# Performance work log

Hardware: AMD Instinct MI355X
Metric: run time of the kernel (lower is better)

## Reference

```python
import jax, jax.numpy as jnp
import numpy as np

IN_CH, OUT_CH, K, STRIDE, PAD = 256, 256, 3, 1, 1

# Straight-through-estimator sign (torch Binarize: sign fwd, identity bwd)
@jax.custom_vjp
def ste_sign(x):
    return jnp.sign(x)

def _ste_fwd(x):
    return jnp.sign(x), None

def _ste_bwd(_, g):
    return (g,)

ste_sign.defvjp(_ste_fwd, _ste_bwd)


def setup_inputs() -> dict:
    key = jax.random.key(0)
    ks = jax.random.split(key, 4)
    x = jax.random.normal(ks[0], (32, IN_CH, 56, 56), jnp.float32)
    shift1 = jnp.zeros((1, IN_CH, 1, 1), jnp.float32)
    shift2 = jnp.zeros((1, IN_CH, 1, 1), jnp.float32)
    fan_in = IN_CH * K * K
    weight = jax.random.normal(ks[1], (OUT_CH, IN_CH, K, K), jnp.float32) / np.sqrt(fan_in)
    bias = jax.random.normal(ks[2], (OUT_CH,), jnp.float32) * 0.01
    w1 = jax.random.uniform(ks[3], (1,), jnp.float32) * 0.001  # channel_w scalar
    return {"x": x, "shift1": shift1, "shift2": shift2,
            "weight": weight, "bias": bias, "w1": w1}


def _binarize_conv2d(x, weight, bias):
    # BinarizeConv2d: binarize input (in_ch != 3) and weight via sign, fp conv, add bias
    xb = ste_sign(x)
    wb = ste_sign(weight)
    out = jax.lax.conv_general_dilated(
        xb, wb,
        window_strides=(STRIDE, STRIDE),
        padding=[(PAD, PAD), (PAD, PAD)],
        dimension_numbers=("NCHW", "OIHW", "NCHW"))
    return out + bias[None, :, None, None]


def reference(x, shift1, shift2, weight, bias, w1):
    out1 = _binarize_conv2d(x + shift1, weight, bias)
    out2 = _binarize_conv2d(x + shift2, weight, bias)
    return out1 + w1 * out2
```

## Files before the change

kernel.cpp:

```cpp
#include <hip/hip_runtime.h>
#include <stdint.h>

typedef __attribute__((ext_vector_type(4))) int   i32x4v;
typedef __attribute__((ext_vector_type(16))) int  i32x16v;
typedef __attribute__((ext_vector_type(4))) float f32x4;

#define PIX 3136
#define WW 56
#define SLAB 215296
#define APL 3712
#define WIN16 928
#define EPQ (32*69*4)
#define LDSB (4*EPQ)

#define XBP_BYTES ((size_t)32*4*3364*64)
#define OFF_XBP2  (XBP_BYTES)
#define OFF_WBT   (2*XBP_BYTES)
#define WBT_BYTES ((size_t)9*16*256*16)
#define OFF_FLAG  (OFF_WBT + WBT_BYTES)
#define WS_NEED   (OFF_FLAG + 64)

__global__ __launch_bounds__(256) void k_prep(
    const float* __restrict__ s1, const float* __restrict__ s2,
    const float* __restrict__ w, char* __restrict__ ws,
    char* __restrict__ wbTt, int* __restrict__ flag) {
    int b = blockIdx.x;
    int t = threadIdx.x;
    if (b == 0) {
        __shared__ int bad;
        if (t == 0) bad = 0;
        __syncthreads();
        if (s1[t] != s2[t]) atomicAdd(&bad, 1);
        __syncthreads();
        if (t == 0) *flag = (bad == 0) ? 1 : 0;
        return;
    }
    if (b <= 256) {
        char* base = ws + (size_t)(b - 1) * SLAB;
        int4 z = {0, 0, 0, 0};
#pragma unroll
        for (int i = 0; i < 4; ++i) {
            int u = t + i * 256;
            if (u >= 912) break;
            int off;
            if (u < 232)      off = u;
            else if (u < 464) off = 57 * 232 + (u - 232);
            else if (u < 688) { int r = (u - 464) >> 2; off = (r + 1) * 232 + ((u - 464) & 3); }
            else              { int r = (u - 688) >> 2; off = (r + 1) * 232 + 228 + ((u - 688) & 3); }
            *(int4*)(base + off * 16) = z;
        }
        return;
    }
    int idx = (b - 257) * 256 + t;
    int kk = idx >> 16;
    int sub = (idx >> 12) & 15;
    int oc = (idx >> 4) & 255;
    int lo = idx & 15;
    float v = w[(oc * 256 + sub * 16 + lo) * 9 + kk];
    wbTt[idx] = (v > 0.f) ? (char)1 : ((v < 0.f) ? (char)-1 : (char)0);
}

__global__ __launch_bounds__(256) void k_repack_x(
    const float* __restrict__ x, const float* __restrict__ sh1,
    const float* __restrict__ sh2, char* __restrict__ xbp1,
    char* __restrict__ xbp2, const int* __restrict__ flag) {
    __shared__ float lds[64 * 68];
    bool eq = (*flag != 0);
    int t = threadIdx.x;
    int b = blockIdx.x;
    int n = b / 49;
    int p0 = (b % 49) * 64;

    int pixw = t >> 2;
    int sub  = t & 3;
    int pw = p0 + pixw;
    int yw = pw / WW, xw = pw % WW;

    int cl = t >> 4;
    int p4 = (t & 15) * 4;

    for (int cc = 0; cc < 256; cc += 64) {
        __syncthreads();
#pragma unroll
        for (int i = 0; i < 4; ++i) {
            float4 v = *(const float4*)(x + (size_t)(n * 256 + cc + cl + i * 16) * PIX + p0 + p4);
            *(float4*)(&lds[(cl + i * 16) * 68 + p4]) = v;
        }
        __syncthreads();
        size_t obase = (size_t)(n * 4 + (cc >> 6)) * SLAB
                     + ((size_t)(yw + 1) * 58 + (xw + 1)) * 64 + sub * 16;
        union { char c[16]; int4 v; } u1, u2;
#pragma unroll
        for (int k = 0; k < 16; ++k) {
            int c = sub * 16 + k;
            float v = lds[c * 68 + pixw];
            float a1 = v + sh1[cc + c];
            float a2 = v + sh2[cc + c];
            u1.c[k] = (a1 > 0.f) ? (char)1 : ((a1 < 0.f) ? (char)-1 : (char)0);
            u2.c[k] = (a2 > 0.f) ? (char)1 : ((a2 < 0.f) ? (char)-1 : (char)0);
        }
        *(int4*)(xbp1 + obase) = u1.v;
        if (!eq) *(int4*)(xbp2 + obase) = u2.v;
    }
}

template <int MODE>
__global__ __launch_bounds__(256, 3) void k_bgemm(
    const char* __restrict__ xsrc, const char* __restrict__ wbTt,
    const float* __restrict__ bias, const float* __restrict__ w1,
    const int* __restrict__ flag, float* __restrict__ out) {
    bool eq = (*flag != 0);
    if (MODE == 0 ? !eq : eq) return;

    __shared__ char lds[LDSB];

    int t = threadIdx.x;
    int l = t & 63, wid = t >> 6;
    int r32 = l & 31, half = l >> 5;

    int logical = (blockIdx.x & 7) * 196 + (blockIdx.x >> 3);
    int n = logical / 49, tp = logical % 49;
    int p0 = tp * 64;
    int y0 = p0 / WW;
    int ocw = wid * 64;

    int wpm[2];
#pragma unroll
    for (int mi = 0; mi < 2; ++mi) {
        int g = p0 + mi * 32 + r32;
        int yg = g / WW, xg = g - yg * WW;
        wpm[mi] = (yg + 1 - y0) * 58 + xg + 1;
    }

    int4 rA[4];
    i32x4v bf[6][2];

    auto loadRA = [&](int cc_) {
        const char* sb = xsrc + (size_t)(n * 4 + cc_) * SLAB + (size_t)y0 * 3712;
#pragma unroll
        for (int j = 0; j < 4; ++j) {
            int u = t + j * 256;
            if (u < WIN16) rA[j] = *(const int4*)(sb + u * 16);
        }
    };
    auto writeA = [&]() {
#pragma unroll
        for (int j = 0; j < 4; ++j) {
            int u = t + j * 256;
            if (u < WIN16) *(int4*)(lds + (u & 3) * APL + (u >> 2) * 16) = rA[j];
        }
    };
    auto loadB = [&](int rot, int sk) {
        int cc_ = sk / 18, kk_ = (sk / 2) % 9, kq_ = sk & 1;
#pragma unroll
        for (int nj = 0; nj < 2; ++nj)
            bf[rot][nj] = *(const i32x4v*)(wbTt +
                (((size_t)((kk_ * 16 + cc_ * 4 + kq_ * 2 + half) * 256
                           + ocw + nj * 32 + r32)) << 4));
    };

    i32x16v acc[2][2];
#pragma unroll
    for (int mi = 0; mi < 2; ++mi)
#pragma unroll
        for (int nj = 0; nj < 2; ++nj)
#pragma unroll
            for (int i = 0; i < 16; ++i) acc[mi][nj][i] = 0;

    loadRA(0);
    loadB(0, 0); loadB(1, 1); loadB(2, 2); loadB(3, 3); loadB(4, 4);

#pragma unroll
    for (int cc = 0; cc < 4; ++cc) {
        __syncthreads();
        writeA();
        __syncthreads();
#pragma unroll
        for (int kk = 0; kk < 9; ++kk) {
            const int ts = (kk / 3 - 1) * 58 + (kk % 3) - 1;
#pragma unroll
            for (int kq = 0; kq < 2; ++kq) {
                const int sk = cc * 18 + kk * 2 + kq;
                if (sk + 5 < 72) loadB((sk + 5) % 6, sk + 5);
                if (kk == 7 && kq == 1 && cc < 3) loadRA(cc + 1);
                const int ci = kq * 2 + half;
                i32x4v af0 = *(const i32x4v*)(lds + ci * APL + (wpm[0] + ts) * 16);
                i32x4v af1 = *(const i32x4v*)(lds + ci * APL + (wpm[1] + ts) * 16);
                const int cur = sk % 6;
                acc[0][0] = __builtin_amdgcn_mfma_i32_32x32x32_i8(af0, bf[cur][0], acc[0][0], 0, 0, 0);
                acc[0][1] = __builtin_amdgcn_mfma_i32_32x32x32_i8(af0, bf[cur][1], acc[0][1], 0, 0, 0);
                acc[1][0] = __builtin_amdgcn_mfma_i32_32x32x32_i8(af1, bf[cur][0], acc[1][0], 0, 0, 0);
                acc[1][1] = __builtin_amdgcn_mfma_i32_32x32x32_i8(af1, bf[cur][1], acc[1][1], 0, 0, 0);
            }
        }
    }

    __syncthreads();
    float w1v = w1[0];
    float se = 1.f + w1v;
    float* sb = (float*)(lds + wid * EPQ);
    size_t outb = (size_t)n * 256 * PIX + p0;

#pragma unroll
    for (int nj = 0; nj < 2; ++nj) {
        float bv = bias[ocw + nj * 32 + r32];
#pragma unroll
        for (int mi = 0; mi < 2; ++mi)
#pragma unroll
            for (int q = 0; q < 4; ++q) {
                f32x4 v;
#pragma unroll
                for (int j = 0; j < 4; ++j) {
                    float a = (float)(acc[mi][nj][q * 4 + j]);
                    if (MODE == 0)      v[j] = (a + bv) * se;
                    else if (MODE == 1) v[j] = a + se * bv;
                    else                v[j] = w1v * a;
                }
                *(f32x4*)(sb + r32 * 69 + mi * 32 + q * 8 + half * 4) = v;
            }
        asm volatile("s_waitcnt lgkmcnt(0)" ::: "memory");
#pragma unroll
        for (int p = 0; p < 8; ++p) {
            int row = p * 4 + (l >> 4);
            int px4 = (l & 15) * 4;
            f32x4 v = *(const f32x4*)(sb + row * 69 + px4);
            float* op = out + outb + (size_t)(ocw + nj * 32 + row) * PIX + px4;
            if (MODE == 2) {
                f32x4 o = *(const f32x4*)op;
                v[0] += o[0]; v[1] += o[1]; v[2] += o[2]; v[3] += o[3];
            }
            __builtin_nontemporal_store(v, (f32x4*)op);
        }
        if (nj == 0) asm volatile("s_waitcnt lgkmcnt(0)" ::: "memory");
    }
}

extern "C" void kernel_launch(void* const* d_in, const int* in_sizes, int n_in,
                              void* d_out, int out_size, void* d_ws, size_t ws_size,
                              hipStream_t stream) {
    const float* x    = (const float*)d_in[0];
    const float* sh1  = (const float*)d_in[1];
    const float* sh2  = (const float*)d_in[2];
    const float* wgt  = (const float*)d_in[3];
    const float* bias = (const float*)d_in[4];
    const float* w1   = (const float*)d_in[5];
    float* out = (float*)d_out;
    char* ws = (char*)d_ws;
    if (ws_size < WS_NEED) return;

    char* xbp1 = ws;
    char* xbp2 = ws + OFF_XBP2;
    char* wbTt = ws + OFF_WBT;
    int* flag  = (int*)(ws + OFF_FLAG);

    k_prep<<<2561, 256, 0, stream>>>(sh1, sh2, wgt, ws, wbTt, flag);
    k_repack_x<<<32 * 49, 256, 0, stream>>>(x, sh1, sh2, xbp1, xbp2, flag);
    k_bgemm<0><<<1568, 256, 0, stream>>>(xbp1, wbTt, bias, w1, flag, out);
    k_bgemm<1><<<1568, 256, 0, stream>>>(xbp1, wbTt, bias, w1, flag, out);
    k_bgemm<2><<<1568, 256, 0, stream>>>(xbp2, wbTt, bias, w1, flag, out);
}
```

Measured before the change: 120.1 us.

## Double-buffer LDS A-fragment reads and pad LDS plane stride

A fragments are now prefetched from LDS into a two-slot register buffer one MFMA step ahead, so the LDS read latency overlaps the current step's four MFMAs. The LDS per-channel plane stride is also padded from 3712 to 3776 bytes, separate from the global row stride, which is meant to reduce bank conflicts between channel planes. This adds registers and LDS footprint, which may affect occupancy. With the loop fully unrolled, the compiler may already have scheduled these reads early.

Result: no change. 118.5 us (-1.3%).

```diff
diff --git a/kernel.cpp b/kernel.cpp
--- a/kernel.cpp
+++ b/kernel.cpp
@@ -8,7 +8,8 @@
 #define PIX 3136
 #define WW 56
 #define SLAB 215296
-#define APL 3712
+#define GROW 3712
+#define APL 3776
 #define WIN16 928
 #define EPQ (32*69*4)
 #define LDSB (4*EPQ)
@@ -134,9 +135,10 @@
 
     int4 rA[4];
     i32x4v bf[6][2];
+    i32x4v afb[2][2];
 
     auto loadRA = [&](int cc_) {
-        const char* sb = xsrc + (size_t)(n * 4 + cc_) * SLAB + (size_t)y0 * 3712;
+        const char* sb = xsrc + (size_t)(n * 4 + cc_) * SLAB + (size_t)y0 * GROW;
 #pragma unroll
         for (int j = 0; j < 4; ++j) {
             int u = t + j * 256;
@@ -175,22 +177,30 @@
         __syncthreads();
         writeA();
         __syncthreads();
+        afb[0][0] = *(const i32x4v*)(lds + half * APL + (wpm[0] - 59) * 16);
+        afb[0][1] = *(const i32x4v*)(lds + half * APL + (wpm[1] - 59) * 16);
 #pragma unroll
         for (int kk = 0; kk < 9; ++kk) {
-            const int ts = (kk / 3 - 1) * 58 + (kk % 3) - 1;
 #pragma unroll
             for (int kq = 0; kq < 2; ++kq) {
-                const int sk = cc * 18 + kk * 2 + kq;
+                const int sl = kk * 2 + kq;
+                const int sk = cc * 18 + sl;
+                const int par = sl & 1;
+                if (sl < 17) {
+                    const int nkk = (sl + 1) >> 1, nkq = (sl + 1) & 1;
+                    const int nts = (nkk / 3 - 1) * 58 + (nkk % 3) - 1;
+                    afb[par ^ 1][0] = *(const i32x4v*)(lds + (nkq * 2 + half) * APL
+                                                       + (wpm[0] + nts) * 16);
+                    afb[par ^ 1][1] = *(const i32x4v*)(lds + (nkq * 2 + half) * APL
+                                                       + (wpm[1] + nts) * 16);
+                }
                 if (sk + 5 < 72) loadB((sk + 5) % 6, sk + 5);
                 if (kk == 7 && kq == 1 && cc < 3) loadRA(cc + 1);
-                const int ci = kq * 2 + half;
-                i32x4v af0 = *(const i32x4v*)(lds + ci * APL + (wpm[0] + ts) * 16);
-                i32x4v af1 = *(const i32x4v*)(lds + ci * APL + (wpm[1] + ts) * 16);
                 const int cur = sk % 6;
-                acc[0][0] = __builtin_amdgcn_mfma_i32_32x32x32_i8(af0, bf[cur][0], acc[0][0], 0, 0, 0);
-                acc[0][1] = __builtin_amdgcn_mfma_i32_32x32x32_i8(af0, bf[cur][1], acc[0][1], 0, 0, 0);
-                acc[1][0] = __builtin_amdgcn_mfma_i32_32x32x32_i8(af1, bf[cur][0], acc[1][0], 0, 0, 0);
-                acc[1][1] = __builtin_amdgcn_mfma_i32_32x32x32_i8(af1, bf[cur][1], acc[1][1], 0, 0, 0);
+                acc[0][0] = __builtin_amdgcn_mfma_i32_32x32x32_i8(afb[par][0], bf[cur][0], acc[0][0], 0, 0, 0);
+                acc[0][1] = __builtin_amdgcn_mfma_i32_32x32x32_i8(afb[par][0], bf[cur][1], acc[0][1], 0, 0, 0);
+                acc[1][0] = __builtin_amdgcn_mfma_i32_32x32x32_i8(afb[par][1], bf[cur][0], acc[1][0], 0, 0, 0);
+                acc[1][1] = __builtin_amdgcn_mfma_i32_32x32x32_i8(afb[par][1], bf[cur][1], acc[1][1], 0, 0, 0);
             }
         }
     }
```

## Stage activations and weights into LDS via direct global-to-LDS double buffering

Applied to the files above, without the earlier changes.

Changes the packed activation layout from pixel-interleaved channel groups to per-subgroup planes, so each wave can copy a contiguous window straight into LDS. Both the activation window and the per-tap weight tile are now double-buffered in LDS through global_load_lds, replacing register-staged A copies and per-lane register prefetch of B. The aim is to cut VGPR pressure and overlap global loads with MFMA work. In exchange it adds a barrier after every tap, uses 64KB of LDS, and lowers the launch bound from 3 to 2 waves per SIMD, which reduces occupancy.

Measured after the change: 116.6 us. -2.9%, faster.

```diff
diff --git a/kernel.cpp b/kernel.cpp
--- a/kernel.cpp
+++ b/kernel.cpp
@@ -7,13 +7,13 @@
 
 #define PIX 3136
 #define WW 56
+#define SPL 53824
 #define SLAB 215296
-#define APL 3712
-#define WIN16 928
+#define ABUF 16384
 #define EPQ (32*69*4)
-#define LDSB (4*EPQ)
-
-#define XBP_BYTES ((size_t)32*4*3364*64)
+#define LDSB 65536
+
+#define XBP_BYTES ((size_t)32*4*215296)
 #define OFF_XBP2  (XBP_BYTES)
 #define OFF_WBT   (2*XBP_BYTES)
 #define WBT_BYTES ((size_t)9*16*256*16)
@@ -42,12 +42,12 @@
         for (int i = 0; i < 4; ++i) {
             int u = t + i * 256;
             if (u >= 912) break;
+            int s = u / 228, v = u - s * 228;
             int off;
-            if (u < 232)      off = u;
-            else if (u < 464) off = 57 * 232 + (u - 232);
-            else if (u < 688) { int r = (u - 464) >> 2; off = (r + 1) * 232 + ((u - 464) & 3); }
-            else              { int r = (u - 688) >> 2; off = (r + 1) * 232 + 228 + ((u - 688) & 3); }
-            *(int4*)(base + off * 16) = z;
+            if (v < 58)       off = v;
+            else if (v < 116) off = 3306 + (v - 58);
+            else { int r = v - 116; off = ((r >> 1) + 1) * 58 + (r & 1) * 57; }
+            *(int4*)(base + s * SPL + off * 16) = z;
         }
         return;
     }
@@ -87,8 +87,8 @@
             *(float4*)(&lds[(cl + i * 16) * 68 + p4]) = v;
         }
         __syncthreads();
-        size_t obase = (size_t)(n * 4 + (cc >> 6)) * SLAB
-                     + ((size_t)(yw + 1) * 58 + (xw + 1)) * 64 + sub * 16;
+        size_t obase = (size_t)(n * 4 + (cc >> 6)) * SLAB + (size_t)sub * SPL
+                     + ((size_t)(yw + 1) * 58 + (xw + 1)) * 16;
         union { char c[16]; int4 v; } u1, u2;
 #pragma unroll
         for (int k = 0; k < 16; ++k) {
@@ -105,7 +105,7 @@
 }
 
 template <int MODE>
-__global__ __launch_bounds__(256, 3) void k_bgemm(
+__global__ __launch_bounds__(256, 2) void k_bgemm(
     const char* __restrict__ xsrc, const char* __restrict__ wbTt,
     const float* __restrict__ bias, const float* __restrict__ w1,
     const int* __restrict__ flag, float* __restrict__ out) {
@@ -132,70 +132,62 @@
         wpm[mi] = (yg + 1 - y0) * 58 + xg + 1;
     }
 
-    int4 rA[4];
-    i32x4v bf[6][2];
-
-    auto loadRA = [&](int cc_) {
-        const char* sb = xsrc + (size_t)(n * 4 + cc_) * SLAB + (size_t)y0 * 3712;
-#pragma unroll
-        for (int j = 0; j < 4; ++j) {
-            int u = t + j * 256;
-            if (u < WIN16) rA[j] = *(const int4*)(sb + u * 16);
-        }
+    auto stageB = [&](int par, int t2) {
+        const int cc2 = t2 / 9, kk2 = t2 % 9;
+        const char* src = wbTt + kk2 * 65536 + cc2 * 16384 + wid * 4096 + l * 16;
+        char* dst = lds + 32768 + par * 16384 + wid * 4096;
+#pragma unroll
+        for (int j = 0; j < 4; ++j)
+            __builtin_amdgcn_global_load_lds(
+                (const __attribute__((address_space(1))) void*)(src + j * 1024),
+                (__attribute__((address_space(3))) void*)(dst + j * 1024), 16, 0, 0);
     };
-    auto writeA = [&]() {
-#pragma unroll
-        for (int j = 0; j < 4; ++j) {
-            int u = t + j * 256;
-            if (u < WIN16) *(int4*)(lds + (u & 3) * APL + (u >> 2) * 16) = rA[j];
-        }
+    auto stageA = [&](int par, int cc2) {
+        const char* src = xsrc + (size_t)(n * 4 + cc2) * SLAB + (size_t)wid * SPL
+                        + y0 * 928 + l * 16;
+        char* dst = lds + par * ABUF + wid * 4096;
+#pragma unroll
+        for (int j = 0; j < 4; ++j)
+            __builtin_amdgcn_global_load_lds(
+                (const __attribute__((address_space(1))) void*)(src + j * 1024),
+                (__attribute__((address_space(3))) void*)(dst + j * 1024), 16, 0, 0);
     };
-    auto loadB = [&](int rot, int sk) {
-        int cc_ = sk / 18, kk_ = (sk / 2) % 9, kq_ = sk & 1;
+
+    i32x16v acc[2][2];
+#pragma unroll
+    for (int mi = 0; mi < 2; ++mi)
 #pragma unroll
         for (int nj = 0; nj < 2; ++nj)
-            bf[rot][nj] = *(const i32x4v*)(wbTt +
-                (((size_t)((kk_ * 16 + cc_ * 4 + kq_ * 2 + half) * 256
-                           + ocw + nj * 32 + r32)) << 4));
-    };
-
-    i32x16v acc[2][2];
-#pragma unroll
-    for (int mi = 0; mi < 2; ++mi)
-#pragma unroll
-        for (int nj = 0; nj < 2; ++nj)
 #pragma unroll
             for (int i = 0; i < 16; ++i) acc[mi][nj][i] = 0;
 
-    loadRA(0);
-    loadB(0, 0); loadB(1, 1); loadB(2, 2); loadB(3, 3); loadB(4, 4);
-
-#pragma unroll
-    for (int cc = 0; cc < 4; ++cc) {
-        __syncthreads();
-        writeA();
-        __syncthreads();
-#pragma unroll
-        for (int kk = 0; kk < 9; ++kk) {
-            const int ts = (kk / 3 - 1) * 58 + (kk % 3) - 1;
-#pragma unroll
-            for (int kq = 0; kq < 2; ++kq) {
-                const int sk = cc * 18 + kk * 2 + kq;
-                if (sk + 5 < 72) loadB((sk + 5) % 6, sk + 5);
-                if (kk == 7 && kq == 1 && cc < 3) loadRA(cc + 1);
-                const int ci = kq * 2 + half;
-                i32x4v af0 = *(const i32x4v*)(lds + ci * APL + (wpm[0] + ts) * 16);
-                i32x4v af1 = *(const i32x4v*)(lds + ci * APL + (wpm[1] + ts) * 16);
-                const int cur = sk % 6;
-                acc[0][0] = __builtin_amdgcn_mfma_i32_32x32x32_i8(af0, bf[cur][0], acc[0][0], 0, 0, 0);
-                acc[0][1] = __builtin_amdgcn_mfma_i32_32x32x32_i8(af0, bf[cur][1], acc[0][1], 0, 0, 0);
-                acc[1][0] = __builtin_amdgcn_mfma_i32_32x32x32_i8(af1, bf[cur][0], acc[1][0], 0, 0, 0);
-                acc[1][1] = __builtin_amdgcn_mfma_i32_32x32x32_i8(af1, bf[cur][1], acc[1][1], 0, 0, 0);
-            }
-        }
-    }
-
+    stageA(0, 0);
+    stageB(0, 0);
     __syncthreads();
+
+#pragma unroll
+    for (int tix = 0; tix < 36; ++tix) {
+        const int cc = tix / 9, kk = tix % 9;
+        if (tix < 35) stageB((tix + 1) & 1, tix + 1);
+        if (kk == 4 && cc < 3) stageA((cc + 1) & 1, cc + 1);
+        const int ts = (kk / 3 - 1) * 58 + (kk % 3) - 1;
+        const char* Ab = lds + (cc & 1) * ABUF;
+        const char* Bb = lds + 32768 + (tix & 1) * 16384;
+#pragma unroll
+        for (int kq = 0; kq < 2; ++kq) {
+            const int ci = kq * 2 + half;
+            i32x4v af0 = *(const i32x4v*)(Ab + ci * 4096 + (wpm[0] + ts) * 16);
+            i32x4v af1 = *(const i32x4v*)(Ab + ci * 4096 + (wpm[1] + ts) * 16);
+            i32x4v bf0 = *(const i32x4v*)(Bb + ci * 4096 + (ocw + r32) * 16);
+            i32x4v bf1 = *(const i32x4v*)(Bb + ci * 4096 + (ocw + 32 + r32) * 16);
+            acc[0][0] = __builtin_amdgcn_mfma_i32_32x32x32_i8(af0, bf0, acc[0][0], 0, 0, 0);
+            acc[0][1] = __builtin_amdgcn_mfma_i32_32x32x32_i8(af0, bf1, acc[0][1], 0, 0, 0);
+            acc[1][0] = __builtin_amdgcn_mfma_i32_32x32x32_i8(af1, bf0, acc[1][0], 0, 0, 0);
+            acc[1][1] = __builtin_amdgcn_mfma_i32_32x32x32_i8(af1, bf1, acc[1][1], 0, 0, 0);
+        }
+        __syncthreads();
+    }
+
     float w1v = w1[0];
     float se = 1.f + w1v;
     float* sb = (float*)(lds + wid * EPQ);
```
